# Optimization experiments

Measured on AMD Instinct MI355X. Metric: run time of the kernel, lower is better.

Reference implementation:

```python
import math
import jax, jax.numpy as jnp
import numpy as np

NHEAD = 8


def setup_inputs() -> dict:
    key = jax.random.key(0)
    ks = jax.random.split(key, 16)
    B, S, M, Ss, Ksn, D = 8, 512, 8, 16, 16, 512
    f32 = jnp.float32
    w_scale = 0.05
    return {
        "q_temporal": jax.random.normal(ks[0], (B, S, M, D), f32),
        "k_temporal": jax.random.normal(ks[1], (B, S, M, D), f32),
        "v_temporal": jax.random.normal(ks[2], (B, S, M, D), f32),
        "q_static": jax.random.normal(ks[3], (B, Ss, D), f32),
        "k_static": jax.random.normal(ks[4], (B, Ksn, D), f32),
        "v_static": jax.random.normal(ks[5], (B, Ksn, D), f32),
        "mask_temporal": jax.random.randint(ks[6], (B, S, M), 0, 2).astype(jnp.int32),
        "mask_static": jax.random.randint(ks[7], (B, Ksn), 0, 2).astype(jnp.int32),
        "Wq": jax.random.normal(ks[8], (D, D), f32) * w_scale,
        "bq": jax.random.normal(ks[9], (D,), f32) * w_scale,
        "Wk": jax.random.normal(ks[10], (D, D), f32) * w_scale,
        "bk": jax.random.normal(ks[11], (D,), f32) * w_scale,
        "Wv": jax.random.normal(ks[12], (D, D), f32) * w_scale,
        "bv": jax.random.normal(ks[13], (D,), f32) * w_scale,
        "Wo": jax.random.normal(ks[14], (D, D), f32) * w_scale,
        "bo": jax.random.normal(ks[15], (D,), f32) * w_scale,
    }


def reference(q_temporal, k_temporal, v_temporal, q_static, k_static, v_static,
              mask_temporal, mask_static, Wq, bq, Wk, bk, Wv, bv, Wo, bo):
    B, S, M, D = q_temporal.shape
    dh = D // NHEAD
    scale = 1.0 / math.sqrt(dh)
    SM = S * M

    def lin(x, W, b):
        return x @ W + b

    def h5(x):  # [B,S,M,D] -> [B,H,S,M,dh]
        b, s, m, d = x.shape
        return x.reshape(b, s, m, NHEAD, dh).transpose(0, 3, 1, 2, 4)

    def h4(x):  # [B,N,D] -> [B,H,N,dh]
        b, n, d = x.shape
        return x.reshape(b, n, NHEAD, dh).transpose(0, 2, 1, 3)

    # additive masks: 1 -> 0 (keep), 0 -> -inf
    m_t = jnp.where(mask_temporal == 1, 0.0, -jnp.inf)  # [B,S,M]
    m_s = jnp.where(mask_static == 1, 0.0, -jnp.inf)    # [B,Ks]

    # shared static-key/value heads: [B,H,Ks,dh]
    Ks_h = h4(lin(k_static, Wk, bk))
    Vs_h = h4(lin(v_static, Wv, bv))

    # ---- temporal side ----
    Qt = h5(lin(q_temporal, Wq, bq))   # [B,H,S,M,dh]
    Kt = h5(lin(k_temporal, Wk, bk))
    Vt = h5(lin(v_temporal, Wv, bv))
    qt_kt = jnp.einsum('bhsmd,bhsnd->bhsmn', Qt, Kt) * scale + m_t[:, None, :, None, :]   # [B,H,S,M,M]
    qt_ks = jnp.einsum('bhsmd,bhkd->bhsmk', Qt, Ks_h) * scale + m_s[:, None, None, None, :]  # [B,H,S,M,Ks]
    w_t = jax.nn.softmax(jnp.concatenate([qt_kt, qt_ks], axis=-1), axis=-1)  # [B,H,S,M,M+Ks]
    qkv_t = (jnp.einsum('bhsmn,bhsnd->bhsmd', w_t[..., :M], Vt)
             + jnp.einsum('bhsmk,bhkd->bhsmd', w_t[..., M:], Vs_h))          # [B,H,S,M,dh]
    out_t = lin(qkv_t.transpose(0, 2, 3, 1, 4).reshape(B, S, M, D), Wo, bo)  # [B,S,M,D]

    # ---- static side ----
    Qs = h4(lin(q_static, Wq, bq))                              # [B,H,Ss,dh]
    Kt_f = h4(lin(k_temporal.reshape(B, SM, D), Wk, bk))        # [B,H,S*M,dh]
    Vt_f = h4(lin(v_temporal.reshape(B, SM, D), Wv, bv))
    qs_kt = jnp.einsum('bhqd,bhnd->bhqn', Qs, Kt_f) * scale + m_t.reshape(B, 1, 1, SM)  # [B,H,Ss,S*M]
    qs_ks = jnp.einsum('bhqd,bhkd->bhqk', Qs, Ks_h) * scale + m_s[:, None, None, :]     # [B,H,Ss,Ks]
    w_s = jax.nn.softmax(jnp.concatenate([qs_kt, qs_ks], axis=-1), axis=-1)  # [B,H,Ss,S*M+Ks]
    qkv_s = (jnp.einsum('bhqn,bhnd->bhqd', w_s[..., :SM], Vt_f)
             + jnp.einsum('bhqk,bhkd->bhqd', w_s[..., SM:], Vs_h))           # [B,H,Ss,dh]
    Ss = qkv_s.shape[2]
    out_s = lin(qkv_s.transpose(0, 2, 1, 3).reshape(B, Ss, D), Wo, bo)       # [B,Ss,D]

    return (out_t, w_t, out_s, w_s)
```

## Files before the change

### kernel.cpp

```cpp
#include <hip/hip_runtime.h>
#include <hip/hip_bf16.h>

typedef __attribute__((ext_vector_type(8))) __bf16 bf16x8;
typedef __attribute__((ext_vector_type(4))) float f32x4;

__device__ __forceinline__ float b2f(unsigned short u) {
    unsigned int x = ((unsigned int)u) << 16;
    float f;
    __builtin_memcpy(&f, &x, 4);
    return f;
}
__device__ __forceinline__ unsigned short f2b(float f) {
    __hip_bfloat16 h = __float2bfloat16(f);
    unsigned short u;
    __builtin_memcpy(&u, &h, 2);
    return u;
}
union U4 { uint4 v; unsigned short u[8]; };

__global__ __launch_bounds__(256) void transpose512cvt4(
    const float* __restrict__ i0, const float* __restrict__ i1,
    const float* __restrict__ i2, const float* __restrict__ i3,
    unsigned short* __restrict__ o0, unsigned short* __restrict__ o1,
    unsigned short* __restrict__ o2, unsigned short* __restrict__ o3)
{
    const float* in = i0;
    unsigned short* out = o0;
    if (blockIdx.z == 1) { in = i1; out = o1; }
    else if (blockIdx.z == 2) { in = i2; out = o2; }
    else if (blockIdx.z == 3) { in = i3; out = o3; }
    __shared__ float tile[32][33];
    int tx = threadIdx.x & 31, ty = threadIdx.x >> 5;
    int bx = blockIdx.x, by = blockIdx.y;
    #pragma unroll
    for (int i = 0; i < 32; i += 8)
        tile[ty + i][tx] = in[(size_t)(bx * 32 + ty + i) * 512 + by * 32 + tx];
    __syncthreads();
    #pragma unroll
    for (int i = 0; i < 32; i += 8)
        out[(size_t)(by * 32 + ty + i) * 512 + bx * 32 + tx] = f2b(tile[tx][ty + i]);
}

#define GPAD 40

struct GemmSet {
    const void* A;
    const unsigned short* B;
    const float* bias;
    void* C;
    int cmode;
};

template<bool AF32>
__global__ __launch_bounds__(256) void gemm128(
    GemmSet s0, GemmSet s1, GemmSet s2, int M, int N)
{
    GemmSet S = s0;
    if (blockIdx.y == 1) S = s1;
    else if (blockIdx.y == 2) S = s2;

    const int K = 512;
    __shared__ __align__(16) unsigned short As[128 * GPAD];
    __shared__ __align__(16) unsigned short Bs[128 * GPAD];

    int nblk = gridDim.x, bid = blockIdx.x;
    int wid = ((nblk & 7) == 0) ? ((bid & 7) * (nblk >> 3) + (bid >> 3)) : bid;
    int nt = N >> 7;
    int m0 = (wid / nt) * 128, n0 = (wid % nt) * 128;

    int t = threadIdx.x;
    int wave = t >> 6, lane = t & 63, quad = lane >> 4, l16 = lane & 15;
    int wr = wave >> 1, wc = wave & 1;

    f32x4 acc[4][4];
    #pragma unroll
    for (int i = 0; i < 4; ++i)
        #pragma unroll
        for (int j = 0; j < 4; ++j) acc[i][j] = (f32x4){0.f, 0.f, 0.f, 0.f};

    int r = t >> 1, half = (t & 1) * 16;
    const float* Ap32 = (const float*)S.A + (size_t)(m0 + r) * K + half;
    const unsigned short* Ap16 = (const unsigned short*)S.A + (size_t)(m0 + r) * K + half;
    const unsigned short* Bp = S.B + (size_t)(n0 + r) * K + half;

    float4 fa0, fa1, fa2, fa3; U4 ua0, ua1; uint4 fb0, fb1;
    float4 ga0, ga1, ga2, ga3; U4 va0, va1; uint4 gb0, gb1;

    auto LOAD0 = [&](int k0) {
        if constexpr (AF32) {
            const float4* p = (const float4*)(Ap32 + k0);
            fa0 = p[0]; fa1 = p[1]; fa2 = p[2]; fa3 = p[3];
        } else {
            ua0.v = *(const uint4*)(Ap16 + k0);
            ua1.v = *(const uint4*)(Ap16 + k0 + 8);
        }
        fb0 = *(const uint4*)(Bp + k0);
        fb1 = *(const uint4*)(Bp + k0 + 8);
    };
    auto LOAD1 = [&](int k0) {
        if constexpr (AF32) {
            const float4* p = (const float4*)(Ap32 + k0);
            ga0 = p[0]; ga1 = p[1]; ga2 = p[2]; ga3 = p[3];
        } else {
            va0.v = *(const uint4*)(Ap16 + k0);
            va1.v = *(const uint4*)(Ap16 + k0 + 8);
        }
        gb0 = *(const uint4*)(Bp + k0);
        gb1 = *(const uint4*)(Bp + k0 + 8);
    };
    auto STORE0 = [&]() {
        U4 a0, a1;
        if constexpr (AF32) {
            a0.u[0]=f2b(fa0.x); a0.u[1]=f2b(fa0.y); a0.u[2]=f2b(fa0.z); a0.u[3]=f2b(fa0.w);
            a0.u[4]=f2b(fa1.x); a0.u[5]=f2b(fa1.y); a0.u[6]=f2b(fa1.z); a0.u[7]=f2b(fa1.w);
            a1.u[0]=f2b(fa2.x); a1.u[1]=f2b(fa2.y); a1.u[2]=f2b(fa2.z); a1.u[3]=f2b(fa2.w);
            a1.u[4]=f2b(fa3.x); a1.u[5]=f2b(fa3.y); a1.u[6]=f2b(fa3.z); a1.u[7]=f2b(fa3.w);
        } else { a0 = ua0; a1 = ua1; }
        *(uint4*)&As[r * GPAD + half] = a0.v;
        *(uint4*)&As[r * GPAD + half + 8] = a1.v;
        *(uint4*)&Bs[r * GPAD + half] = fb0;
        *(uint4*)&Bs[r * GPAD + half + 8] = fb1;
    };
    auto STORE1 = [&]() {
        U4 a0, a1;
        if constexpr (AF32) {
            a0.u[0]=f2b(ga0.x); a0.u[1]=f2b(ga0.y); a0.u[2]=f2b(ga0.z); a0.u[3]=f2b(ga0.w);
            a0.u[4]=f2b(ga1.x); a0.u[5]=f2b(ga1.y); a0.u[6]=f2b(ga1.z); a0.u[7]=f2b(ga1.w);
            a1.u[0]=f2b(ga2.x); a1.u[1]=f2b(ga2.y); a1.u[2]=f2b(ga2.z); a1.u[3]=f2b(ga2.w);
            a1.u[4]=f2b(ga3.x); a1.u[5]=f2b(ga3.y); a1.u[6]=f2b(ga3.z); a1.u[7]=f2b(ga3.w);
        } else { a0 = va0; a1 = va1; }
        *(uint4*)&As[r * GPAD + half] = a0.v;
        *(uint4*)&As[r * GPAD + half + 8] = a1.v;
        *(uint4*)&Bs[r * GPAD + half] = gb0;
        *(uint4*)&Bs[r * GPAD + half + 8] = gb1;
    };
    auto COMPUTE = [&]() {
        bf16x8 af[4], bf[4];
        #pragma unroll
        for (int i = 0; i < 4; ++i)
            af[i] = *(const bf16x8*)&As[(wr * 64 + i * 16 + l16) * GPAD + quad * 8];
        #pragma unroll
        for (int j = 0; j < 4; ++j)
            bf[j] = *(const bf16x8*)&Bs[(wc * 64 + j * 16 + l16) * GPAD + quad * 8];
        #pragma unroll
        for (int i = 0; i < 4; ++i)
            #pragma unroll
            for (int j = 0; j < 4; ++j)
                acc[i][j] = __builtin_amdgcn_mfma_f32_16x16x32_bf16(af[i], bf[j], acc[i][j], 0, 0, 0);
    };

    LOAD0(0);
    LOAD1(32);
    for (int it = 0; it < 16; it += 2) {
        __syncthreads();
        STORE0();
        __syncthreads();
        if (it + 2 < 16) LOAD0((it + 2) * 32);
        COMPUTE();
        __syncthreads();
        STORE1();
        __syncthreads();
        if (it + 3 < 16) LOAD1((it + 3) * 32);
        COMPUTE();
    }

    int cmode = S.cmode;
    #pragma unroll
    for (int i = 0; i < 4; ++i) {
        #pragma unroll
        for (int j = 0; j < 4; ++j) {
            int row = m0 + wr * 64 + i * 16 + quad * 4;
            int col = n0 + wc * 64 + j * 16 + l16;
            float bc = S.bias[col];
            #pragma unroll
            for (int ii = 0; ii < 4; ++ii) {
                float v = acc[i][j][ii] + bc;
                int R = row + ii;
                if (cmode == 0) {
                    ((float*)S.C)[(size_t)R * N + col] = v;
                } else if (cmode == 1) {
                    ((unsigned short*)S.C)[(size_t)R * N + col] = f2b(v);
                } else {
                    int bb = R >> 12, n = R & 4095, hh = col >> 6, d = col & 63;
                    ((unsigned short*)S.C)[(((size_t)bb * 8 + hh) * 4096 + n) * 64 + d] = f2b(v);
                }
            }
        }
    }
}

__global__ __launch_bounds__(512) void temporal_attn(
    const unsigned short* __restrict__ Qt, const unsigned short* __restrict__ KH,
    const unsigned short* __restrict__ VH, const unsigned short* __restrict__ Ksp,
    const unsigned short* __restrict__ Vsp,
    const int* __restrict__ mask_t, const int* __restrict__ mask_s,
    float* __restrict__ w_t_out, unsigned short* __restrict__ qkv_t)
{
    int blk = blockIdx.x;
    int b = blk >> 8, sp = blk & 255;
    int s0 = sp * 2;
    int t = threadIdx.x;
    int h = t >> 6, lane = t & 63, quad = lane >> 4, l16 = lane & 15;

    __shared__ __align__(16) unsigned short Vt[8][64 * 40];
    __shared__ __align__(16) unsigned short Pl[8][16 * 40];

    size_t bh = (size_t)(b * 8 + h);
    size_t tok0 = ((size_t)(b * 512 + s0)) * 8;

    {
        int r = lane & 31, dh = (lane >> 5) * 32;
        const unsigned short* src = (r < 16)
            ? VH + (bh * 4096 + (size_t)(s0 * 8 + r)) * 64 + dh
            : Vsp + ((size_t)(b * 16 + (r - 16))) * 512 + h * 64 + dh;
        U4 u[4];
        #pragma unroll
        for (int g = 0; g < 4; ++g) u[g].v = ((const uint4*)src)[g];
        unsigned short* dst = &Vt[h][0];
        #pragma unroll
        for (int g = 0; g < 4; ++g)
            #pragma unroll
            for (int ii = 0; ii < 8; ++ii)
                dst[(dh + g * 8 + ii) * 40 + r] = u[g].u[ii];
    }

    const unsigned short* qp = Qt + (tok0 + l16) * 512 + h * 64 + quad * 8;
    bf16x8 qf0 = *(const bf16x8*)qp;
    bf16x8 qf1 = *(const bf16x8*)(qp + 32);
    const unsigned short* kpt = KH + (bh * 4096 + (size_t)(s0 * 8 + l16)) * 64 + quad * 8;
    bf16x8 kt0 = *(const bf16x8*)kpt;
    bf16x8 kt1 = *(const bf16x8*)(kpt + 32);
    const unsigned short* kps = Ksp + ((size_t)(b * 16 + l16)) * 512 + h * 64 + quad * 8;
    bf16x8 ks0 = *(const bf16x8*)kps;
    bf16x8 ks1 = *(const bf16x8*)(kps + 32);

    f32x4 sc0 = (f32x4){0.f, 0.f, 0.f, 0.f};
    f32x4 sc1 = (f32x4){0.f, 0.f, 0.f, 0.f};
    sc0 = __builtin_amdgcn_mfma_f32_16x16x32_bf16(qf0, kt0, sc0, 0, 0, 0);
    sc0 = __builtin_amdgcn_mfma_f32_16x16x32_bf16(qf1, kt1, sc0, 0, 0, 0);
    sc1 = __builtin_amdgcn_mfma_f32_16x16x32_bf16(qf0, ks0, sc1, 0, 0, 0);
    sc1 = __builtin_amdgcn_mfma_f32_16x16x32_bf16(qf1, ks1, sc1, 0, 0, 0);

    float madd0 = mask_t[tok0 + l16] ? 0.f : -1e30f;
    bool v0 = ((quad < 2) == (l16 < 8));
    if (!v0) madd0 = -1e30f;
    float madd1 = mask_s[b * 16 + l16] ? 0.f : -1e30f;

    float w0[4], w1[4];
    #pragma unroll
    for (int i = 0; i < 4; ++i) {
        float a = sc0[i] * 0.125f + madd0;
        float c = sc1[i] * 0.125f + madd1;
        float mx = fmaxf(a, c);
        mx = fmaxf(mx, __shfl_xor(mx, 1));
        mx = fmaxf(mx, __shfl_xor(mx, 2));
        mx = fmaxf(mx, __shfl_xor(mx, 4));
        mx = fmaxf(mx, __shfl_xor(mx, 8));
        float e0 = __expf(a - mx), e1 = __expf(c - mx);
        float se = e0 + e1;
        se += __shfl_xor(se, 1);
        se += __shfl_xor(se, 2);
        se += __shfl_xor(se, 4);
        se += __shfl_xor(se, 8);
        float inv = 1.f / se;
        w0[i] = e0 * inv;
        w1[i] = e1 * inv;
    }

    int row0 = quad * 4;
    #pragma unroll
    for (int i = 0; i < 4; ++i) {
        int row = row0 + i;
        Pl[h][row * 40 + l16] = f2b(w0[i]);
        Pl[h][row * 40 + 16 + l16] = f2b(w1[i]);
        int s = s0 + (row >> 3), m = row & 7;
        size_t wb = ((((size_t)b * 8 + h) * 512 + s) * 8 + m) * 24;
        if (v0) w_t_out[wb + (l16 & 7)] = w0[i];
        w_t_out[wb + 8 + l16] = w1[i];
    }

    bf16x8 pa = *(const bf16x8*)&Pl[h][l16 * 40 + quad * 8];
    f32x4 oacc[4];
    #pragma unroll
    for (int j = 0; j < 4; ++j) {
        bf16x8 vb = *(const bf16x8*)&Vt[h][(j * 16 + l16) * 40 + quad * 8];
        oacc[j] = (f32x4){0.f, 0.f, 0.f, 0.f};
        oacc[j] = __builtin_amdgcn_mfma_f32_16x16x32_bf16(pa, vb, oacc[j], 0, 0, 0);
    }
    #pragma unroll
    for (int j = 0; j < 4; ++j)
        #pragma unroll
        for (int ii = 0; ii < 4; ++ii) {
            int row = quad * 4 + ii;
            qkv_t[(tok0 + row) * 512 + h * 64 + j * 16 + l16] = f2b(oacc[j][ii]);
        }
}

__global__ __launch_bounds__(256) void static_attn_s1(
    const unsigned short* __restrict__ Qsp, const unsigned short* __restrict__ KH,
    const unsigned short* __restrict__ VH, const unsigned short* __restrict__ Ksp,
    const unsigned short* __restrict__ Vsp,
    const int* __restrict__ mask_t, const int* __restrict__ mask_s,
    float* __restrict__ w_s, float* __restrict__ Ppart, float* __restrict__ Lpart)
{
    int blk = blockIdx.x;
    int bh = blk & 63, c = blk >> 6;
    int b = bh >> 3, h = bh & 7;
    __shared__ __align__(16) unsigned short Klds[32 * 72];
    __shared__ __align__(16) unsigned short Vlds[64 * 40];
    __shared__ __align__(16) unsigned short Plds[16 * 40];
    __shared__ float maskv[32];
    __shared__ float sL[2][16];
    int t = threadIdx.x, wave = t >> 6, lane = t & 63, quad = lane >> 4, l16 = lane & 15;

    bf16x8 qf0 = *(const bf16x8*)(Qsp + ((size_t)(b * 16 + l16)) * 512 + h * 64 + quad * 8);
    bf16x8 qf1 = *(const bf16x8*)(Qsp + ((size_t)(b * 16 + l16)) * 512 + h * 64 + 32 + quad * 8);

    f32x4 pacc = (f32x4){0.f, 0.f, 0.f, 0.f};
    float Lacc[4] = {0.f, 0.f, 0.f, 0.f};
    int d0 = wave * 16;
    int sub = wave >> 1;
    int sr = t >> 3, spart = t & 7;
    int s0 = c * 16, s1 = (c == 7) ? 129 : (s0 + 16);

    for (int st = s0; st < s1; ++st) {
        int key0 = st * 32;
        int kk = key0 + sr;
        uint4 kv = {0, 0, 0, 0}, vv = {0, 0, 0, 0};
        if (kk < 4096) {
            kv = *(const uint4*)(KH + (((size_t)bh) * 4096 + kk) * 64 + spart * 8);
            vv = *(const uint4*)(VH + (((size_t)bh) * 4096 + kk) * 64 + spart * 8);
        } else if (kk < 4112) {
            kv = *(const uint4*)(Ksp + ((size_t)(b * 16 + kk - 4096)) * 512 + h * 64 + spart * 8);
            vv = *(const uint4*)(Vsp + ((size_t)(b * 16 + kk - 4096)) * 512 + h * 64 + spart * 8);
        }
        __syncthreads();
        *(uint4*)&Klds[sr * 72 + spart * 8] = kv;
        {
            U4 u; u.v = vv;
            #pragma unroll
            for (int ii = 0; ii < 8; ++ii) Vlds[(spart * 8 + ii) * 40 + sr] = u.u[ii];
        }
        if (t < 32) {
            int k2 = key0 + t;
            float ma = -1e30f;
            if (k2 < 4096) ma = mask_t[b * 4096 + k2] ? 0.f : -1e30f;
            else if (k2 < 4112) ma = mask_s[b * 16 + k2 - 4096] ? 0.f : -1e30f;
            maskv[t] = ma;
        }
        __syncthreads();
        if ((wave & 1) == 0) {
            bf16x8 kf0 = *(const bf16x8*)&Klds[(sub * 16 + l16) * 72 + quad * 8];
            bf16x8 kf1 = *(const bf16x8*)&Klds[(sub * 16 + l16) * 72 + 32 + quad * 8];
            f32x4 sc = (f32x4){0.f, 0.f, 0.f, 0.f};
            sc = __builtin_amdgcn_mfma_f32_16x16x32_bf16(qf0, kf0, sc, 0, 0, 0);
            sc = __builtin_amdgcn_mfma_f32_16x16x32_bf16(qf1, kf1, sc, 0, 0, 0);
            float ma = maskv[sub * 16 + l16];
            size_t wbase = (((size_t)bh) * 16 + quad * 4) * 4112 + key0 + sub * 16 + l16;
            #pragma unroll
            for (int i = 0; i < 4; ++i) {
                float sv = sc[i] * 0.125f + ma;
                float w = __expf(sv);
                Lacc[i] += w;
                w_s[wbase + (size_t)i * 4112] = w;
                Plds[(quad * 4 + i) * 40 + sub * 16 + l16] = f2b(w);
            }
        }
        __syncthreads();
        bf16x8 pf = *(const bf16x8*)&Plds[l16 * 40 + quad * 8];
        bf16x8 vf = *(const bf16x8*)&Vlds[(d0 + l16) * 40 + quad * 8];
        pacc = __builtin_amdgcn_mfma_f32_16x16x32_bf16(pf, vf, pacc, 0, 0, 0);
    }

    if ((wave & 1) == 0) {
        #pragma unroll
        for (int i = 0; i < 4; ++i) {
            float v = Lacc[i];
            v += __shfl_xor(v, 1);
            v += __shfl_xor(v, 2);
            v += __shfl_xor(v, 4);
            v += __shfl_xor(v, 8);
            Lacc[i] = v;
        }
        if (l16 == 0) {
            #pragma unroll
            for (int i = 0; i < 4; ++i) sL[wave >> 1][quad * 4 + i] = Lacc[i];
        }
    }
    size_t pbase = ((size_t)(bh * 8 + c) * 16 + quad * 4) * 64 + d0 + l16;
    #pragma unroll
    for (int i = 0; i < 4; ++i) Ppart[pbase + (size_t)i * 64] = pacc[i];
    __syncthreads();
    if (t < 16) Lpart[(bh * 8 + c) * 16 + t] = sL[0][t] + sL[1][t];
}

__global__ __launch_bounds__(256) void static_attn_s4(
    const float* __restrict__ Ppart, const float* __restrict__ Lpart,
    float* __restrict__ w_s, unsigned short* __restrict__ qkvS)
{
    int bh = blockIdx.x, b = bh >> 3, h = bh & 7;
    __shared__ float invL[16];
    int t = threadIdx.x;
    if (t < 16) {
        float L = 0.f;
        #pragma unroll
        for (int cc = 0; cc < 8; ++cc) L += Lpart[(bh * 8 + cc) * 16 + t];
        invL[t] = 1.f / L;
    }
    __syncthreads();
    #pragma unroll
    for (int i = 0; i < 4; ++i) {
        int idx = t + i * 256;
        int q = idx >> 6, d = idx & 63;
        float s = 0.f;
        #pragma unroll
        for (int cc = 0; cc < 8; ++cc) s += Ppart[((size_t)(bh * 8 + cc) * 16 + q) * 64 + d];
        qkvS[((size_t)(b * 16 + q)) * 512 + h * 64 + d] = f2b(s * invL[q]);
    }
    size_t base = (size_t)bh * 16 * 4112;
    for (int q = 0; q < 16; ++q) {
        float il = invL[q];
        for (int kk = t; kk < 4112; kk += 256) w_s[base + q * 4112 + kk] *= il;
    }
}

extern "C" void kernel_launch(void* const* d_in, const int* in_sizes, int n_in,
                              void* d_out, int out_size, void* d_ws, size_t ws_size,
                              hipStream_t stream)
{
    const float* q_t = (const float*)d_in[0];
    const float* k_t = (const float*)d_in[1];
    const float* v_t = (const float*)d_in[2];
    const float* q_s = (const float*)d_in[3];
    const float* k_s = (const float*)d_in[4];
    const float* v_s = (const float*)d_in[5];
    const int* m_t = (const int*)d_in[6];
    const int* m_s = (const int*)d_in[7];
    const float* Wq = (const float*)d_in[8];
    const float* bq = (const float*)d_in[9];
    const float* Wk = (const float*)d_in[10];
    const float* bk = (const float*)d_in[11];
    const float* Wv = (const float*)d_in[12];
    const float* bv = (const float*)d_in[13];
    const float* Wo = (const float*)d_in[14];
    const float* bo = (const float*)d_in[15];

    char* ws = (char*)d_ws;
    size_t off = 0;
    auto alloc = [&](size_t bytes) {
        void* p = ws + off;
        off += (bytes + 255) & ~(size_t)255;
        return p;
    };
    const size_t WB = (size_t)512 * 512 * 2;
    const size_t TB = (size_t)32768 * 512 * 2;
    const size_t SB = (size_t)128 * 512 * 2;
    unsigned short* WqT = (unsigned short*)alloc(WB);
    unsigned short* WkT = (unsigned short*)alloc(WB);
    unsigned short* WvT = (unsigned short*)alloc(WB);
    unsigned short* WoT = (unsigned short*)alloc(WB);
    unsigned short* Qt   = (unsigned short*)alloc(TB);
    unsigned short* KH   = (unsigned short*)alloc(TB);
    unsigned short* VH   = (unsigned short*)alloc(TB);
    unsigned short* qkvT = (unsigned short*)alloc(TB);
    unsigned short* Qsp  = (unsigned short*)alloc(SB);
    unsigned short* Ksp  = (unsigned short*)alloc(SB);
    unsigned short* Vsp  = (unsigned short*)alloc(SB);
    unsigned short* qkvS = (unsigned short*)alloc(SB);
    float* Ppart = (float*)alloc((size_t)64 * 8 * 16 * 64 * 4);
    float* Lpart = (float*)alloc((size_t)64 * 8 * 16 * 4);

    float* out    = (float*)d_out;
    float* out_tp = out;
    float* w_t_o  = out + 16777216;
    float* out_sp = out + 23068672;
    float* w_s_o  = out + 23134208;

    transpose512cvt4<<<dim3(16, 16, 4), 256, 0, stream>>>(Wq, Wk, Wv, Wo, WqT, WkT, WvT, WoT);

    GemmSet gq  = { q_t,  WqT, bq, Qt,   1 };
    GemmSet gk  = { k_t,  WkT, bk, KH,   2 };
    GemmSet gv  = { v_t,  WvT, bv, VH,   2 };
    GemmSet gqs = { q_s,  WqT, bq, Qsp,  1 };
    GemmSet gks = { k_s,  WkT, bk, Ksp,  1 };
    GemmSet gvs = { v_s,  WvT, bv, Vsp,  1 };
    GemmSet got = { qkvT, WoT, bo, out_tp, 0 };
    GemmSet gos = { qkvS, WoT, bo, out_sp, 0 };

    gemm128<true><<<dim3(1024, 3), 256, 0, stream>>>(gq, gk, gv, 32768, 512);
    gemm128<true><<<dim3(4, 3),    256, 0, stream>>>(gqs, gks, gvs, 128, 512);

    temporal_attn<<<2048, 512, 0, stream>>>(Qt, KH, VH, Ksp, Vsp, m_t, m_s, w_t_o, qkvT);
    static_attn_s1<<<512, 256, 0, stream>>>(Qsp, KH, VH, Ksp, Vsp, m_t, m_s, w_s_o, Ppart, Lpart);
    static_attn_s4<<<64, 256, 0, stream>>>(Ppart, Lpart, w_s_o, qkvS);

    gemm128<false><<<dim3(1024, 1), 256, 0, stream>>>(got, got, got, 32768, 512);
    gemm128<false><<<dim3(4, 1),    256, 0, stream>>>(gos, gos, gos, 128, 512);
}
```

Measured before the change: 581.3 us.

## Restructure projection GEMMs: stage half of B in LDS, stream A directly into registers

Replaces the 128x128 double-buffered LDS GEMM with a 512-thread kernel in which each wave owns 64 rows of A, loaded straight from global memory into MFMA registers, while a 128x256 slice of the transposed weight is staged in XOR-swizzled LDS in two phases. Each block now computes a 512x128 output tile. This removes the A-tile LDS round trip and most barriers and raises reuse of the weight tile. In exchange the A loads are strided per lane with no coalescing through LDS, the kernel needs 64 KB of LDS and more accumulator registers, and the grid is smaller with a new block-to-tile mapping.

```diff
diff --git a/kernel.cpp b/kernel.cpp
--- a/kernel.cpp
+++ b/kernel.cpp
@@ -41,7 +41,6 @@
         out[(size_t)(by * 32 + ty + i) * 512 + bx * 32 + tx] = f2b(tile[tx][ty + i]);
 }
 
-#define GPAD 40
 
 struct GemmSet {
     const void* A;
@@ -52,126 +51,121 @@
 };
 
 template<bool AF32>
-__global__ __launch_bounds__(256) void gemm128(
-    GemmSet s0, GemmSet s1, GemmSet s2, int M, int N)
-{
-    GemmSet S = s0;
-    if (blockIdx.y == 1) S = s1;
-    else if (blockIdx.y == 2) S = s2;
-
-    const int K = 512;
-    __shared__ __align__(16) unsigned short As[128 * GPAD];
-    __shared__ __align__(16) unsigned short Bs[128 * GPAD];
-
-    int nblk = gridDim.x, bid = blockIdx.x;
-    int wid = ((nblk & 7) == 0) ? ((bid & 7) * (nblk >> 3) + (bid >> 3)) : bid;
-    int nt = N >> 7;
-    int m0 = (wid / nt) * 128, n0 = (wid % nt) * 128;
+__global__ __launch_bounds__(512, 2) void gemm_bp(
+    GemmSet s0, GemmSet s1, GemmSet s2, int M, int mgroups)
+{
+    const int K = 512, N = 512;
+    __shared__ __align__(16) unsigned short Bs[128 * 256];
+
+    int NB = gridDim.x, bid = blockIdx.x;
+    int wid;
+    if ((NB & 31) == 0) {
+        int x = bid & 7, tt = bid >> 3, r = tt & 3, j = tt >> 2;
+        wid = (j * 8 + x) * 4 + r;
+    } else wid = bid;
+    int q = wid >> 2, np = wid & 3;
+    int g = q / mgroups, mg = q - g * mgroups;
+    GemmSet S = (g == 0) ? s0 : ((g == 1) ? s1 : s2);
+    int n0 = np * 128, m0 = mg * 512;
 
     int t = threadIdx.x;
-    int wave = t >> 6, lane = t & 63, quad = lane >> 4, l16 = lane & 15;
-    int wr = wave >> 1, wc = wave & 1;
-
-    f32x4 acc[4][4];
+    int w = t >> 6, lane = t & 63, quad = lane >> 4, l16 = lane & 15;
+    bool active = (m0 + w * 64) < M;
+    size_t mrow = (size_t)(m0 + w * 64 + l16);
+
+    const float* Ap32 = (const float*)S.A + mrow * K + quad * 8;
+    const unsigned short* Ap16 = (const unsigned short*)S.A + mrow * K + quad * 8;
+
+    int srow = t >> 2, sseg = t & 3;
+    const unsigned short* Bg = S.B + (size_t)(n0 + srow) * K + sseg * 64;
+    char* Bsb = (char*)Bs;
+    unsigned int wbase = ((unsigned int)srow << 9) + ((unsigned int)sseg << 7);
+    unsigned int wxor = ((unsigned int)(srow & 7)) << 4;
+    unsigned int rxor = ((unsigned int)(l16 & 7)) << 4;
+
+    f32x4 acc[4][8];
     #pragma unroll
     for (int i = 0; i < 4; ++i)
         #pragma unroll
-        for (int j = 0; j < 4; ++j) acc[i][j] = (f32x4){0.f, 0.f, 0.f, 0.f};
-
-    int r = t >> 1, half = (t & 1) * 16;
-    const float* Ap32 = (const float*)S.A + (size_t)(m0 + r) * K + half;
-    const unsigned short* Ap16 = (const unsigned short*)S.A + (size_t)(m0 + r) * K + half;
-    const unsigned short* Bp = S.B + (size_t)(n0 + r) * K + half;
-
-    float4 fa0, fa1, fa2, fa3; U4 ua0, ua1; uint4 fb0, fb1;
-    float4 ga0, ga1, ga2, ga3; U4 va0, va1; uint4 gb0, gb1;
-
-    auto LOAD0 = [&](int k0) {
+        for (int j = 0; j < 8; ++j) acc[i][j] = (f32x4){0.f, 0.f, 0.f, 0.f};
+
+    float4 pf[8];
+    uint4 ph[4];
+
+    auto ALOAD = [&](int kk) {
         if constexpr (AF32) {
-            const float4* p = (const float4*)(Ap32 + k0);
-            fa0 = p[0]; fa1 = p[1]; fa2 = p[2]; fa3 = p[3];
+            #pragma unroll
+            for (int i = 0; i < 4; ++i) {
+                const float4* pp = (const float4*)(Ap32 + (size_t)i * 16 * K + kk);
+                pf[2 * i] = pp[0]; pf[2 * i + 1] = pp[1];
+            }
         } else {
-            ua0.v = *(const uint4*)(Ap16 + k0);
-            ua1.v = *(const uint4*)(Ap16 + k0 + 8);
-        }
-        fb0 = *(const uint4*)(Bp + k0);
-        fb1 = *(const uint4*)(Bp + k0 + 8);
+            #pragma unroll
+            for (int i = 0; i < 4; ++i)
+                ph[i] = *(const uint4*)(Ap16 + (size_t)i * 16 * K + kk);
+        }
     };
-    auto LOAD1 = [&](int k0) {
+    auto ACVT = [&](bf16x8* af) {
         if constexpr (AF32) {
-            const float4* p = (const float4*)(Ap32 + k0);
-            ga0 = p[0]; ga1 = p[1]; ga2 = p[2]; ga3 = p[3];
+            #pragma unroll
+            for (int i = 0; i < 4; ++i) {
+                U4 u;
+                u.u[0] = f2b(pf[2*i].x);   u.u[1] = f2b(pf[2*i].y);
+                u.u[2] = f2b(pf[2*i].z);   u.u[3] = f2b(pf[2*i].w);
+                u.u[4] = f2b(pf[2*i+1].x); u.u[5] = f2b(pf[2*i+1].y);
+                u.u[6] = f2b(pf[2*i+1].z); u.u[7] = f2b(pf[2*i+1].w);
+                af[i] = *(bf16x8*)&u;
+            }
         } else {
-            va0.v = *(const uint4*)(Ap16 + k0);
-            va1.v = *(const uint4*)(Ap16 + k0 + 8);
-        }
-        gb0 = *(const uint4*)(Bp + k0);
-        gb1 = *(const uint4*)(Bp + k0 + 8);
+            #pragma unroll
+            for (int i = 0; i < 4; ++i) af[i] = *(bf16x8*)&ph[i];
+        }
     };
-    auto STORE0 = [&]() {
-        U4 a0, a1;
-        if constexpr (AF32) {
-            a0.u[0]=f2b(fa0.x); a0.u[1]=f2b(fa0.y); a0.u[2]=f2b(fa0.z); a0.u[3]=f2b(fa0.w);
-            a0.u[4]=f2b(fa1.x); a0.u[5]=f2b(fa1.y); a0.u[6]=f2b(fa1.z); a0.u[7]=f2b(fa1.w);
-            a1.u[0]=f2b(fa2.x); a1.u[1]=f2b(fa2.y); a1.u[2]=f2b(fa2.z); a1.u[3]=f2b(fa2.w);
-            a1.u[4]=f2b(fa3.x); a1.u[5]=f2b(fa3.y); a1.u[6]=f2b(fa3.z); a1.u[7]=f2b(fa3.w);
-        } else { a0 = ua0; a1 = ua1; }
-        *(uint4*)&As[r * GPAD + half] = a0.v;
-        *(uint4*)&As[r * GPAD + half + 8] = a1.v;
-        *(uint4*)&Bs[r * GPAD + half] = fb0;
-        *(uint4*)&Bs[r * GPAD + half + 8] = fb1;
+    auto STAGE = [&](int p) {
+        uint4 v[8];
+        #pragma unroll
+        for (int i = 0; i < 8; ++i)
+            v[i] = *(const uint4*)(Bg + p * 256 + i * 8);
+        #pragma unroll
+        for (int i = 0; i < 8; ++i)
+            *(uint4*)(Bsb + ((wbase + i * 16) ^ wxor)) = v[i];
     };
-    auto STORE1 = [&]() {
-        U4 a0, a1;
-        if constexpr (AF32) {
-            a0.u[0]=f2b(ga0.x); a0.u[1]=f2b(ga0.y); a0.u[2]=f2b(ga0.z); a0.u[3]=f2b(ga0.w);
-            a0.u[4]=f2b(ga1.x); a0.u[5]=f2b(ga1.y); a0.u[6]=f2b(ga1.z); a0.u[7]=f2b(ga1.w);
-            a1.u[0]=f2b(ga2.x); a1.u[1]=f2b(ga2.y); a1.u[2]=f2b(ga2.z); a1.u[3]=f2b(ga2.w);
-            a1.u[4]=f2b(ga3.x); a1.u[5]=f2b(ga3.y); a1.u[6]=f2b(ga3.z); a1.u[7]=f2b(ga3.w);
-        } else { a0 = va0; a1 = va1; }
-        *(uint4*)&As[r * GPAD + half] = a0.v;
-        *(uint4*)&As[r * GPAD + half + 8] = a1.v;
-        *(uint4*)&Bs[r * GPAD + half] = gb0;
-        *(uint4*)&Bs[r * GPAD + half + 8] = gb1;
-    };
-    auto COMPUTE = [&]() {
-        bf16x8 af[4], bf[4];
-        #pragma unroll
-        for (int i = 0; i < 4; ++i)
-            af[i] = *(const bf16x8*)&As[(wr * 64 + i * 16 + l16) * GPAD + quad * 8];
-        #pragma unroll
-        for (int j = 0; j < 4; ++j)
-            bf[j] = *(const bf16x8*)&Bs[(wc * 64 + j * 16 + l16) * GPAD + quad * 8];
-        #pragma unroll
-        for (int i = 0; i < 4; ++i)
-            #pragma unroll
-            for (int j = 0; j < 4; ++j)
-                acc[i][j] = __builtin_amdgcn_mfma_f32_16x16x32_bf16(af[i], bf[j], acc[i][j], 0, 0, 0);
-    };
-
-    LOAD0(0);
-    LOAD1(32);
-    for (int it = 0; it < 16; it += 2) {
+
+    if (active) ALOAD(0);
+    #pragma unroll
+    for (int p = 0; p < 2; ++p) {
         __syncthreads();
-        STORE0();
+        STAGE(p);
         __syncthreads();
-        if (it + 2 < 16) LOAD0((it + 2) * 32);
-        COMPUTE();
-        __syncthreads();
-        STORE1();
-        __syncthreads();
-        if (it + 3 < 16) LOAD1((it + 3) * 32);
-        COMPUTE();
-    }
-
+        if (active) {
+            int kb = p * 256;
+            for (int ks = 0; ks < 8; ++ks) {
+                bf16x8 af[4];
+                ACVT(af);
+                if (ks < 7) ALOAD(kb + (ks + 1) * 32);
+                else if (p == 0) ALOAD(256);
+                unsigned int kl2b = (unsigned int)((ks * 32 + quad * 8) * 2);
+                #pragma unroll
+                for (int j = 0; j < 8; ++j) {
+                    unsigned int rb = (((unsigned int)(j * 16 + l16)) << 9) + kl2b;
+                    bf16x8 bf = *(const bf16x8*)(Bsb + (rb ^ rxor));
+                    #pragma unroll
+                    for (int i = 0; i < 4; ++i)
+                        acc[i][j] = __builtin_amdgcn_mfma_f32_16x16x32_bf16(af[i], bf, acc[i][j], 0, 0, 0);
+                }
+            }
+        }
+    }
+
+    if (!active) return;
     int cmode = S.cmode;
     #pragma unroll
-    for (int i = 0; i < 4; ++i) {
-        #pragma unroll
-        for (int j = 0; j < 4; ++j) {
-            int row = m0 + wr * 64 + i * 16 + quad * 4;
-            int col = n0 + wc * 64 + j * 16 + l16;
-            float bc = S.bias[col];
+    for (int j = 0; j < 8; ++j) {
+        int col = n0 + j * 16 + l16;
+        float bc = S.bias[col];
+        #pragma unroll
+        for (int i = 0; i < 4; ++i) {
+            int row = m0 + w * 64 + i * 16 + quad * 4;
             #pragma unroll
             for (int ii = 0; ii < 4; ++ii) {
                 float v = acc[i][j][ii] + bc;
@@ -487,13 +481,13 @@
     GemmSet got = { qkvT, WoT, bo, out_tp, 0 };
     GemmSet gos = { qkvS, WoT, bo, out_sp, 0 };
 
-    gemm128<true><<<dim3(1024, 3), 256, 0, stream>>>(gq, gk, gv, 32768, 512);
-    gemm128<true><<<dim3(4, 3),    256, 0, stream>>>(gqs, gks, gvs, 128, 512);
+    gemm_bp<true><<<dim3(768), 512, 0, stream>>>(gq, gk, gv, 32768, 64);
+    gemm_bp<true><<<dim3(12), 512, 0, stream>>>(gqs, gks, gvs, 128, 1);
 
     temporal_attn<<<2048, 512, 0, stream>>>(Qt, KH, VH, Ksp, Vsp, m_t, m_s, w_t_o, qkvT);
     static_attn_s1<<<512, 256, 0, stream>>>(Qsp, KH, VH, Ksp, Vsp, m_t, m_s, w_s_o, Ppart, Lpart);
     static_attn_s4<<<64, 256, 0, stream>>>(Ppart, Lpart, w_s_o, qkvS);
 
-    gemm128<false><<<dim3(1024, 1), 256, 0, stream>>>(got, got, got, 32768, 512);
-    gemm128<false><<<dim3(4, 1),    256, 0, stream>>>(gos, gos, gos, 128, 512);
-}
+    gemm_bp<false><<<dim3(256), 512, 0, stream>>>(got, got, got, 32768, 64);
+    gemm_bp<false><<<dim3(4), 512, 0, stream>>>(gos, gos, gos, 128, 1);
+}
```

Result: no change. 582.7 us (+0.2%).
